# Kernel tuning notes

Hardware: AMD Instinct MI355X
Metric: run time of the kernel (lower is better)

## Reference

```python
import jax, jax.numpy as jnp
import numpy as np

N0, N1, N2 = 200000, 100000, 50000
E0, E1 = 1600000, 800000
IN_F, H_F, N_CLS = 128, 256, 64


def sage_conv(h_src, src_idx, dst_idx, num_dst, W_self, W_neigh, b):
    # DGL SAGEConv with aggregator_type='mean':
    #   h_neigh = mean over in-neighbors of h_src
    #   out = h_dst @ W_self + h_neigh @ W_neigh + b
    h_dst = h_src[:num_dst]
    msgs = h_src[src_idx]                                   # [E, F] gather
    summed = jax.ops.segment_sum(msgs, dst_idx, num_segments=num_dst)
    deg = jax.ops.segment_sum(jnp.ones((src_idx.shape[0],), h_src.dtype),
                              dst_idx, num_segments=num_dst)
    h_neigh = summed / jnp.maximum(deg, 1.0)[:, None]       # mean, safe for deg=0
    return h_dst @ W_self + h_neigh @ W_neigh + b


def setup_inputs() -> dict:
    key = jax.random.key(0)
    ks = jax.random.split(key, 10)
    s1 = 1.0 / np.sqrt(IN_F)
    s2 = 1.0 / np.sqrt(H_F)
    return {
        "x": jax.random.normal(ks[0], (N0, IN_F), jnp.float32),
        "src0": jax.random.randint(ks[1], (E0,), 0, N0, jnp.int64 if jax.config.jax_enable_x64 else jnp.int32),
        "dst0": jnp.sort(jax.random.randint(ks[2], (E0,), 0, N1)),
        "src1": jax.random.randint(ks[3], (E1,), 0, N1),
        "dst1": jnp.sort(jax.random.randint(ks[4], (E1,), 0, N2)),
        "num_dst0": N1,
        "num_dst1": N2,
        "W_self1": jax.random.normal(ks[5], (IN_F, H_F), jnp.float32) * s1,
        "W_neigh1": jax.random.normal(ks[6], (IN_F, H_F), jnp.float32) * s1,
        "b1": jnp.zeros((H_F,), jnp.float32),
        "W_self2": jax.random.normal(ks[7], (H_F, N_CLS), jnp.float32) * s2,
        "W_neigh2": jax.random.normal(ks[8], (H_F, N_CLS), jnp.float32) * s2,
        "b2": jnp.zeros((N_CLS,), jnp.float32),
    }


def reference(x, src0, dst0, src1, dst1, num_dst0, num_dst1,
              W_self1, W_neigh1, b1, W_self2, W_neigh2, b2):
    h = sage_conv(x, src0, dst0, num_dst0, W_self1, W_neigh1, b1)   # [N1, H]
    h = jax.nn.relu(h)
    h = sage_conv(h, src1, dst1, num_dst1, W_self2, W_neigh2, b2)   # [N2, C]
    return h
```

## Files before the change

kernel.cpp:

```cpp
#include <hip/hip_runtime.h>

constexpr int cN0  = 200000;
constexpr int cN1  = 100000;
constexpr int cN2  = 50000;
constexpr int cE0  = 1600000;
constexpr int cE1  = 800000;
constexpr int cIN  = 128;
constexpr int cH   = 256;
constexpr int cCLS = 64;

constexpr float QSTEP = 6.0f / 127.0f;
constexpr float QINV  = 127.0f / 6.0f;

using bf16x8 = __attribute__((ext_vector_type(8))) short;
using f32x4  = __attribute__((ext_vector_type(4))) float;

__device__ __forceinline__ float bflo(unsigned int u) {
    union { unsigned int i; float f; } v; v.i = u << 16; return v.f;
}
__device__ __forceinline__ float bfhi(unsigned int u) {
    union { unsigned int i; float f; } v; v.i = u & 0xFFFF0000u; return v.f;
}
__device__ __forceinline__ unsigned int f2bf(float f) {
    union { float f; unsigned int i; } v; v.f = f;
    return (v.i + 0x7FFFu + ((v.i >> 16) & 1u)) >> 16;
}

constexpr int XBLK = (cN0 * cIN / 8) / 256;
constexpr int WCNT = cH * cH + 2 * cCLS * cH;
constexpr int WBLK = WCNT / 256;
constexpr int RCNT = (cN1 + 1) + (cN2 + 1);
constexpr int RBLK = (RCNT + 255) / 256;

__global__ __launch_bounds__(256) void prep(
        const float* __restrict__ x,
        const float* __restrict__ Ws1, const float* __restrict__ Wn1,
        const float* __restrict__ Wn2, const float* __restrict__ Ws2,
        const int* __restrict__ dst0, const int* __restrict__ dst1,
        unsigned short* __restrict__ xb, unsigned int* __restrict__ xq,
        unsigned short* __restrict__ Wt1, unsigned short* __restrict__ Wt2,
        int* __restrict__ row0, int* __restrict__ row1) {
    const int b = blockIdx.x, tid = threadIdx.x;
    if (b < XBLK) {
        const int i = b * 256 + tid;
        const float4* p = (const float4*)x + (size_t)i * 2;
        float4 a = p[0], c = p[1];
        uint4 o;
        o.x = f2bf(a.x) | (f2bf(a.y) << 16);
        o.y = f2bf(a.z) | (f2bf(a.w) << 16);
        o.z = f2bf(c.x) | (f2bf(c.y) << 16);
        o.w = f2bf(c.z) | (f2bf(c.w) << 16);
        ((uint4*)xb)[i] = o;
        auto q8 = [](float v) -> unsigned int {
            int q = __float2int_rn(v * QINV);
            q = q > 127 ? 127 : (q < -127 ? -127 : q);
            return (unsigned int)q & 255u;
        };
        uint2 d;
        d.x = q8(a.x) | (q8(a.y) << 8) | (q8(a.z) << 16) | (q8(a.w) << 24);
        d.y = q8(c.x) | (q8(c.y) << 8) | (q8(c.z) << 16) | (q8(c.w) << 24);
        ((uint2*)xq)[i] = d;
    } else if (b < XBLK + WBLK) {
        const int wi = (b - XBLK) * 256 + tid;
        if (wi < cH * cH) {
            int n = wi >> 8, k = wi & 255;
            float v = (k < cIN) ? Ws1[k * cH + n] : Wn1[(k - cIN) * cH + n];
            Wt1[n * cH + k] = (unsigned short)f2bf(v);
        } else {
            int j = wi - cH * cH; int n = j >> 8, k = j & 255;
            float v = (n < cCLS) ? Wn2[k * cCLS + n] : Ws2[k * cCLS + (n - cCLS)];
            Wt2[n * cH + k] = (unsigned short)f2bf(v);
        }
    } else {
        const int ti = (b - XBLK - WBLK) * 256 + tid;
        if (ti <= cN1) {
            int lo = 0, hi = cE0;
            while (lo < hi) { int mid = (lo + hi) >> 1; if (dst0[mid] < ti) lo = mid + 1; else hi = mid; }
            row0[ti] = lo;
        } else {
            int d = ti - (cN1 + 1);
            if (d <= cN2) {
                int lo = 0, hi = cE1;
                while (lo < hi) { int mid = (lo + hi) >> 1; if (dst1[mid] < d) lo = mid + 1; else hi = mid; }
                row1[d] = lo;
            }
        }
    }
}

__global__ __launch_bounds__(256) void agg_i8(
        const uint2* __restrict__ xq,
        const int* __restrict__ sidx,
        const int* __restrict__ rows,
        unsigned short* __restrict__ nb,
        int num_dst) {
    const int tid = threadIdx.x, lane = tid & 63;
    const int m = blockIdx.x * 4 + (tid >> 6);
    if (m >= num_dst) return;
    const int sub = lane >> 4, t = lane & 15;
    const int e0 = rows[m], e1 = rows[m + 1];

    int acc[8];
    #pragma unroll
    for (int j = 0; j < 8; ++j) acc[j] = 0;
    auto addq = [&](uint2 v) {
        #pragma unroll
        for (int d = 0; d < 2; ++d) {
            unsigned int w = (&v.x)[d];
            acc[d * 4 + 0] += (int)(signed char)(w);
            acc[d * 4 + 1] += (int)(signed char)(w >> 8);
            acc[d * 4 + 2] += (int)(signed char)(w >> 16);
            acc[d * 4 + 3] += (int)(signed char)(w >> 24);
        }
    };

    int base = e0;
    for (; base + 16 <= e1; base += 16) {
        int sA = sidx[base + sub];
        int sB = sidx[base + 4 + sub];
        int sC = sidx[base + 8 + sub];
        int sD = sidx[base + 12 + sub];
        uint2 vA = xq[(size_t)sA * 16 + t];
        uint2 vB = xq[(size_t)sB * 16 + t];
        uint2 vC = xq[(size_t)sC * 16 + t];
        uint2 vD = xq[(size_t)sD * 16 + t];
        addq(vA); addq(vB); addq(vC); addq(vD);
    }
    for (; base < e1; base += 4) {
        int idx = base + sub;
        if (idx < e1) addq(xq[(size_t)sidx[idx] * 16 + t]);
    }

    #pragma unroll
    for (int j = 0; j < 8; ++j) {
        acc[j] += __shfl_xor(acc[j], 16, 64);
        acc[j] += __shfl_xor(acc[j], 32, 64);
    }

    if (sub == 0) {
        const int deg = e1 - e0;
        const float f = QSTEP / (float)(deg > 1 ? deg : 1);
        uint4 w;
        w.x = f2bf(acc[0] * f) | (f2bf(acc[1] * f) << 16);
        w.y = f2bf(acc[2] * f) | (f2bf(acc[3] * f) << 16);
        w.z = f2bf(acc[4] * f) | (f2bf(acc[5] * f) << 16);
        w.w = f2bf(acc[6] * f) | (f2bf(acc[7] * f) << 16);
        ((uint4*)nb)[(size_t)m * 16 + t] = w;
    }
}

template<int K, bool ACCUM>
__global__ __launch_bounds__(256) void agg_wave(
        const unsigned short* __restrict__ src,
        const int* __restrict__ sidx,
        const int* __restrict__ rows,
        void* __restrict__ outv, int num_dst) {
    constexpr int LPR = K / 8;
    constexpr int EPW = 64 / LPR;
    const int tid = threadIdx.x;
    const int lane = tid & 63;
    const int m = blockIdx.x * 4 + (tid >> 6);
    if (m >= num_dst) return;
    const int sub = lane / LPR;
    const int t   = lane % LPR;

    const uint4* s4 = (const uint4*)src;
    const int e0 = rows[m], e1 = rows[m + 1];

    float acc[8];
    #pragma unroll
    for (int j = 0; j < 8; ++j) acc[j] = 0.f;
    auto addv = [&](uint4 v) {
        acc[0] += bflo(v.x); acc[1] += bfhi(v.x);
        acc[2] += bflo(v.y); acc[3] += bfhi(v.y);
        acc[4] += bflo(v.z); acc[5] += bfhi(v.z);
        acc[6] += bflo(v.w); acc[7] += bfhi(v.w);
    };

    int base = e0;
    for (; base + 2 * EPW <= e1; base += 2 * EPW) {
        int sA = sidx[base + sub], sB = sidx[base + EPW + sub];
        uint4 vA = s4[(size_t)sA * LPR + t];
        uint4 vB = s4[(size_t)sB * LPR + t];
        addv(vA); addv(vB);
    }
    for (; base < e1; base += EPW) {
        int idx = base + sub;
        if (idx < e1) addv(s4[(size_t)sidx[idx] * LPR + t]);
    }

    #pragma unroll
    for (int j = 0; j < 8; ++j) {
        #pragma unroll
        for (int off = LPR; off < 64; off <<= 1)
            acc[j] += __shfl_xor(acc[j], off, 64);
    }

    if (sub == 0) {
        const int deg = e1 - e0;
        const float inv = 1.0f / (float)(deg > 1 ? deg : 1);
        if (!ACCUM) {
            uint4 o;
            o.x = f2bf(acc[0] * inv) | (f2bf(acc[1] * inv) << 16);
            o.y = f2bf(acc[2] * inv) | (f2bf(acc[3] * inv) << 16);
            o.z = f2bf(acc[4] * inv) | (f2bf(acc[5] * inv) << 16);
            o.w = f2bf(acc[6] * inv) | (f2bf(acc[7] * inv) << 16);
            ((uint4*)outv)[(size_t)m * LPR + t] = o;
        } else {
            float* op = (float*)outv + (size_t)m * K + t * 8;
            float4 o0 = *(float4*)op, o1 = *(float4*)(op + 4);
            o0.x += acc[0] * inv; o0.y += acc[1] * inv;
            o0.z += acc[2] * inv; o0.w += acc[3] * inv;
            o1.x += acc[4] * inv; o1.y += acc[5] * inv;
            o1.z += acc[6] * inv; o1.w += acc[7] * inv;
            *(float4*)op = o0; *(float4*)(op + 4) = o1;
        }
    }
}

template<int BM, int BN, int WM, int WN, bool RELU, bool HASBIAS, bool OUTBF16>
__global__ __launch_bounds__(256) void gemm_mfma(
        const unsigned short* __restrict__ A1, int K1,
        const unsigned short* __restrict__ A2, int K2,
        const unsigned short* __restrict__ Bt,
        const float* __restrict__ bias,
        void* __restrict__ Cout, int M, int N) {
    static_assert(2 * WM * 16 == BM && 2 * WN * 16 == BN, "wave tiling");
    __shared__ unsigned short As[BM][40];
    __shared__ unsigned short Bs[BN][40];

    const int tid = threadIdx.x;
    const int m0 = blockIdx.x * BM, n0 = blockIdx.y * BN;
    const int lane = tid & 63, wave = tid >> 6;
    const int wrow = wave >> 1, wcol = wave & 1;
    const int quad = lane >> 4, l16 = lane & 15;
    const int K = K1 + K2;

    f32x4 acc[WM][WN];
    #pragma unroll
    for (int i = 0; i < WM; ++i)
        #pragma unroll
        for (int j = 0; j < WN; ++j)
            acc[i][j] = (f32x4){0.f, 0.f, 0.f, 0.f};

    for (int kb = 0; kb < K; kb += 32) {
        const unsigned short* Ab; int lda, kloc;
        if (kb < K1) { Ab = A1; lda = K1; kloc = kb; }
        else         { Ab = A2; lda = K2; kloc = kb - K1; }

        #pragma unroll
        for (int f = 0; f < (BM * 4) / 256; ++f) {
            int idx = tid + f * 256;
            int row = idx >> 2, q = idx & 3;
            int gm = m0 + row;
            uint4 v = make_uint4(0, 0, 0, 0);
            if (gm < M) v = *(const uint4*)(Ab + (size_t)gm * lda + kloc + q * 8);
            *(uint4*)&As[row][q * 8] = v;
        }
        #pragma unroll
        for (int f = 0; f < (BN * 4) / 256; ++f) {
            int idx = tid + f * 256;
            int row = idx >> 2, q = idx & 3;
            uint4 v = *(const uint4*)(Bt + (size_t)(n0 + row) * K + kb + q * 8);
            *(uint4*)&Bs[row][q * 8] = v;
        }
        __syncthreads();

        bf16x8 a[WM], b[WN];
        #pragma unroll
        for (int i = 0; i < WM; ++i)
            a[i] = *(const bf16x8*)&As[(wrow * WM + i) * 16 + l16][quad * 8];
        #pragma unroll
        for (int j = 0; j < WN; ++j)
            b[j] = *(const bf16x8*)&Bs[(wcol * WN + j) * 16 + l16][quad * 8];
        #pragma unroll
        for (int i = 0; i < WM; ++i)
            #pragma unroll
            for (int j = 0; j < WN; ++j)
                acc[i][j] = __builtin_amdgcn_mfma_f32_16x16x32_bf16(
                    a[i], b[j], acc[i][j], 0, 0, 0);
        __syncthreads();
    }

    float bv[WN];
    #pragma unroll
    for (int j = 0; j < WN; ++j)
        bv[j] = HASBIAS ? bias[n0 + (wcol * WN + j) * 16 + l16] : 0.f;
    #pragma unroll
    for (int i = 0; i < WM; ++i) {
        #pragma unroll
        for (int r = 0; r < 4; ++r) {
            int gm = m0 + (wrow * WM + i) * 16 + quad * 4 + r;
            if (gm >= M) continue;
            #pragma unroll
            for (int j = 0; j < WN; ++j) {
                int gn = n0 + (wcol * WN + j) * 16 + l16;
                float v = acc[i][j][r] + bv[j];
                if (RELU) v = fmaxf(v, 0.f);
                if (OUTBF16)
                    ((unsigned short*)Cout)[(size_t)gm * N + gn] = (unsigned short)f2bf(v);
                else
                    ((float*)Cout)[(size_t)gm * N + gn] = v;
            }
        }
    }
}

__global__ __launch_bounds__(256) void gemm2_split(
        const unsigned short* __restrict__ A,
        const unsigned short* __restrict__ Bt,
        const float* __restrict__ b2,
        unsigned short* __restrict__ zb,
        float* __restrict__ out) {
    __shared__ unsigned short As[128][40];
    __shared__ unsigned short Bs[128][40];
    const int tid = threadIdx.x;
    const int m0 = blockIdx.x * 128;
    const int lane = tid & 63, wave = tid >> 6;
    const int wrow = wave >> 1, wcol = wave & 1;
    const int quad = lane >> 4, l16 = lane & 15;

    f32x4 acc[4][4];
    #pragma unroll
    for (int i = 0; i < 4; ++i)
        #pragma unroll
        for (int j = 0; j < 4; ++j)
            acc[i][j] = (f32x4){0.f, 0.f, 0.f, 0.f};

    for (int kb = 0; kb < cH; kb += 32) {
        #pragma unroll
        for (int f = 0; f < 2; ++f) {
            int idx = tid + f * 256;
            int row = idx >> 2, q = idx & 3;
            int gm = m0 + row;
            uint4 v = make_uint4(0, 0, 0, 0);
            if (gm < cN1) v = *(const uint4*)(A + (size_t)gm * cH + kb + q * 8);
            *(uint4*)&As[row][q * 8] = v;
        }
        #pragma unroll
        for (int f = 0; f < 2; ++f) {
            int idx = tid + f * 256;
            int row = idx >> 2, q = idx & 3;
            uint4 v = *(const uint4*)(Bt + (size_t)row * cH + kb + q * 8);
            *(uint4*)&Bs[row][q * 8] = v;
        }
        __syncthreads();

        bf16x8 a[4], b[4];
        #pragma unroll
        for (int i = 0; i < 4; ++i)
            a[i] = *(const bf16x8*)&As[(wrow * 4 + i) * 16 + l16][quad * 8];
        #pragma unroll
        for (int j = 0; j < 4; ++j)
            b[j] = *(const bf16x8*)&Bs[(wcol * 4 + j) * 16 + l16][quad * 8];
        #pragma unroll
        for (int i = 0; i < 4; ++i)
            #pragma unroll
            for (int j = 0; j < 4; ++j)
                acc[i][j] = __builtin_amdgcn_mfma_f32_16x16x32_bf16(
                    a[i], b[j], acc[i][j], 0, 0, 0);
        __syncthreads();
    }

    if (wcol == 0) {
        #pragma unroll
        for (int i = 0; i < 4; ++i) {
            #pragma unroll
            for (int r = 0; r < 4; ++r) {
                int gm = m0 + (wrow * 4 + i) * 16 + quad * 4 + r;
                if (gm >= cN1) continue;
                #pragma unroll
                for (int j = 0; j < 4; ++j) {
                    int gn = j * 16 + l16;
                    zb[(size_t)gm * cCLS + gn] = (unsigned short)f2bf(acc[i][j][r]);
                }
            }
        }
    } else {
        float bv[4];
        #pragma unroll
        for (int j = 0; j < 4; ++j) bv[j] = b2[j * 16 + l16];
        #pragma unroll
        for (int i = 0; i < 4; ++i) {
            #pragma unroll
            for (int r = 0; r < 4; ++r) {
                int gm = m0 + (wrow * 4 + i) * 16 + quad * 4 + r;
                if (gm >= cN2) continue;
                #pragma unroll
                for (int j = 0; j < 4; ++j)
                    out[(size_t)gm * cCLS + j * 16 + l16] = acc[i][j][r] + bv[j];
            }
        }
    }
}

extern "C" void kernel_launch(void* const* d_in, const int* in_sizes, int n_in,
                              void* d_out, int out_size, void* d_ws, size_t ws_size,
                              hipStream_t stream) {
    const float* x      = (const float*)d_in[0];
    const int*   src0   = (const int*)d_in[1];
    const int*   dst0   = (const int*)d_in[2];
    const int*   src1   = (const int*)d_in[3];
    const int*   dst1   = (const int*)d_in[4];
    const float* Wself1  = (const float*)d_in[7];
    const float* Wneigh1 = (const float*)d_in[8];
    const float* b1      = (const float*)d_in[9];
    const float* Wself2  = (const float*)d_in[10];
    const float* Wneigh2 = (const float*)d_in[11];
    const float* b2      = (const float*)d_in[12];
    float* out = (float*)d_out;

    char* ws = (char*)d_ws;
    int* row0 = (int*)ws;
    int* row1 = row0 + (cN1 + 1);
    size_t off = (size_t)((cN1 + 1) + (cN2 + 1)) * sizeof(int);
    off = (off + 1023) & ~(size_t)1023;
    unsigned short* xb = (unsigned short*)(ws + off); off += (size_t)cN0 * cIN * 2;
    unsigned int*   xq = (unsigned int*)(ws + off);
    unsigned short* zb = (unsigned short*)(ws + off); off += (size_t)cN0 * cIN;
    unsigned short* nb  = (unsigned short*)(ws + off); off += (size_t)cN1 * cIN * 2;
    unsigned short* h1b = (unsigned short*)(ws + off); off += (size_t)cN1 * cH * 2;
    unsigned short* Wt1 = (unsigned short*)(ws + off); off += (size_t)cH * cH * 2;
    unsigned short* Wt2 = (unsigned short*)(ws + off); off += (size_t)2 * cCLS * cH * 2;

    prep<<<XBLK + WBLK + RBLK, 256, 0, stream>>>(
        x, Wself1, Wneigh1, Wneigh2, Wself2, dst0, dst1,
        xb, xq, Wt1, Wt2, row0, row1);

    agg_i8<<<(cN1 + 3) / 4, 256, 0, stream>>>(
        (const uint2*)xq, src0, row0, nb, cN1);

    gemm_mfma<128, 128, 4, 4, true, true, true>
        <<<dim3((cN1 + 127) / 128, cH / 128), 256, 0, stream>>>(
        xb, cIN, nb, cIN, Wt1, b1, h1b, cN1, cH);

    gemm2_split<<<(cN1 + 127) / 128, 256, 0, stream>>>(h1b, Wt2, b2, zb, out);

    agg_wave<cCLS, true><<<(cN2 + 3) / 4, 256, 0, stream>>>(
        zb, src1, row1, out, cN2);
}
```

Measured before the change: 341.1 us.

## Register-prefetch GEMM tiles with K=64 steps and full-N tile for layer-one GEMM

```diff
diff --git a/kernel.cpp b/kernel.cpp
--- a/kernel.cpp
+++ b/kernel.cpp
@@ -218,89 +218,98 @@
     }
 }
 
-template<int BM, int BN, int WM, int WN, bool RELU, bool HASBIAS, bool OUTBF16>
-__global__ __launch_bounds__(256) void gemm_mfma(
-        const unsigned short* __restrict__ A1, int K1,
-        const unsigned short* __restrict__ A2, int K2,
+__global__ __launch_bounds__(256) void gemm1_big(
+        const unsigned short* __restrict__ xb,
+        const unsigned short* __restrict__ nb,
         const unsigned short* __restrict__ Bt,
         const float* __restrict__ bias,
-        void* __restrict__ Cout, int M, int N) {
-    static_assert(2 * WM * 16 == BM && 2 * WN * 16 == BN, "wave tiling");
-    __shared__ unsigned short As[BM][40];
-    __shared__ unsigned short Bs[BN][40];
+        unsigned short* __restrict__ h1b) {
+    __shared__ unsigned short As[128][72];
+    __shared__ unsigned short Bs[256][72];
 
     const int tid = threadIdx.x;
-    const int m0 = blockIdx.x * BM, n0 = blockIdx.y * BN;
+    const int m0 = blockIdx.x * 128;
     const int lane = tid & 63, wave = tid >> 6;
-    const int wrow = wave >> 1, wcol = wave & 1;
+    const int wr = wave >> 1, wc = wave & 1;
     const int quad = lane >> 4, l16 = lane & 15;
-    const int K = K1 + K2;
-
-    f32x4 acc[WM][WN];
-    #pragma unroll
-    for (int i = 0; i < WM; ++i)
-        #pragma unroll
-        for (int j = 0; j < WN; ++j)
+
+    uint4 pa[4], pb[8];
+    auto loadA = [&](int kb) {
+        const unsigned short* base = (kb < 128) ? xb : nb;
+        const int koff = (kb < 128) ? kb : kb - 128;
+        #pragma unroll
+        for (int f = 0; f < 4; ++f) {
+            int idx = tid + f * 256;
+            int row = idx >> 3, c = idx & 7;
+            int gm = m0 + row; if (gm > cN1 - 1) gm = cN1 - 1;
+            pa[f] = *(const uint4*)(base + (size_t)gm * 128 + koff + c * 8);
+        }
+    };
+    auto loadB = [&](int kb) {
+        #pragma unroll
+        for (int f = 0; f < 8; ++f) {
+            int idx = tid + f * 256;
+            int row = idx >> 3, c = idx & 7;
+            pb[f] = *(const uint4*)(Bt + (size_t)row * 256 + kb + c * 8);
+        }
+    };
+    auto store = [&]() {
+        #pragma unroll
+        for (int f = 0; f < 4; ++f) {
+            int idx = tid + f * 256;
+            *(uint4*)&As[idx >> 3][(idx & 7) * 8] = pa[f];
+        }
+        #pragma unroll
+        for (int f = 0; f < 8; ++f) {
+            int idx = tid + f * 256;
+            *(uint4*)&Bs[idx >> 3][(idx & 7) * 8] = pb[f];
+        }
+    };
+
+    f32x4 acc[4][8];
+    #pragma unroll
+    for (int i = 0; i < 4; ++i)
+        #pragma unroll
+        for (int j = 0; j < 8; ++j)
             acc[i][j] = (f32x4){0.f, 0.f, 0.f, 0.f};
 
-    for (int kb = 0; kb < K; kb += 32) {
-        const unsigned short* Ab; int lda, kloc;
-        if (kb < K1) { Ab = A1; lda = K1; kloc = kb; }
-        else         { Ab = A2; lda = K2; kloc = kb - K1; }
-
-        #pragma unroll
-        for (int f = 0; f < (BM * 4) / 256; ++f) {
-            int idx = tid + f * 256;
-            int row = idx >> 2, q = idx & 3;
-            int gm = m0 + row;
-            uint4 v = make_uint4(0, 0, 0, 0);
-            if (gm < M) v = *(const uint4*)(Ab + (size_t)gm * lda + kloc + q * 8);
-            *(uint4*)&As[row][q * 8] = v;
-        }
-        #pragma unroll
-        for (int f = 0; f < (BN * 4) / 256; ++f) {
-            int idx = tid + f * 256;
-            int row = idx >> 2, q = idx & 3;
-            uint4 v = *(const uint4*)(Bt + (size_t)(n0 + row) * K + kb + q * 8);
-            *(uint4*)&Bs[row][q * 8] = v;
-        }
+    loadA(0); loadB(0);
+    for (int it = 0; it < 4; ++it) {
+        store();
         __syncthreads();
-
-        bf16x8 a[WM], b[WN];
-        #pragma unroll
-        for (int i = 0; i < WM; ++i)
-            a[i] = *(const bf16x8*)&As[(wrow * WM + i) * 16 + l16][quad * 8];
-        #pragma unroll
-        for (int j = 0; j < WN; ++j)
-            b[j] = *(const bf16x8*)&Bs[(wcol * WN + j) * 16 + l16][quad * 8];
-        #pragma unroll
-        for (int i = 0; i < WM; ++i)
-            #pragma unroll
-            for (int j = 0; j < WN; ++j)
-                acc[i][j] = __builtin_amdgcn_mfma_f32_16x16x32_bf16(
-                    a[i], b[j], acc[i][j], 0, 0, 0);
+        if (it < 3) { loadA((it + 1) * 64); loadB((it + 1) * 64); }
+        #pragma unroll
+        for (int kk = 0; kk < 2; ++kk) {
+            bf16x8 a[4], b[8];
+            #pragma unroll
+            for (int i = 0; i < 4; ++i)
+                a[i] = *(const bf16x8*)&As[(wr * 4 + i) * 16 + l16][kk * 32 + quad * 8];
+            #pragma unroll
+            for (int j = 0; j < 8; ++j)
+                b[j] = *(const bf16x8*)&Bs[(wc * 8 + j) * 16 + l16][kk * 32 + quad * 8];
+            #pragma unroll
+            for (int i = 0; i < 4; ++i)
+                #pragma unroll
+                for (int j = 0; j < 8; ++j)
+                    acc[i][j] = __builtin_amdgcn_mfma_f32_16x16x32_bf16(
+                        a[i], b[j], acc[i][j], 0, 0, 0);
+        }
         __syncthreads();
     }
 
-    float bv[WN];
-    #pragma unroll
-    for (int j = 0; j < WN; ++j)
-        bv[j] = HASBIAS ? bias[n0 + (wcol * WN + j) * 16 + l16] : 0.f;
-    #pragma unroll
-    for (int i = 0; i < WM; ++i) {
+    float bv[8];
+    #pragma unroll
+    for (int j = 0; j < 8; ++j) bv[j] = bias[(wc * 8 + j) * 16 + l16];
+    #pragma unroll
+    for (int i = 0; i < 4; ++i) {
         #pragma unroll
         for (int r = 0; r < 4; ++r) {
-            int gm = m0 + (wrow * WM + i) * 16 + quad * 4 + r;
-            if (gm >= M) continue;
-            #pragma unroll
-            for (int j = 0; j < WN; ++j) {
-                int gn = n0 + (wcol * WN + j) * 16 + l16;
-                float v = acc[i][j][r] + bv[j];
-                if (RELU) v = fmaxf(v, 0.f);
-                if (OUTBF16)
-                    ((unsigned short*)Cout)[(size_t)gm * N + gn] = (unsigned short)f2bf(v);
-                else
-                    ((float*)Cout)[(size_t)gm * N + gn] = v;
+            int gm = m0 + (wr * 4 + i) * 16 + quad * 4 + r;
+            if (gm >= cN1) continue;
+            #pragma unroll
+            for (int j = 0; j < 8; ++j) {
+                float v = fmaxf(acc[i][j][r] + bv[j], 0.f);
+                h1b[(size_t)gm * 256 + (wc * 8 + j) * 16 + l16] = (unsigned short)f2bf(v);
             }
         }
     }
@@ -312,13 +321,41 @@
         const float* __restrict__ b2,
         unsigned short* __restrict__ zb,
         float* __restrict__ out) {
-    __shared__ unsigned short As[128][40];
-    __shared__ unsigned short Bs[128][40];
+    __shared__ unsigned short As[128][72];
+    __shared__ unsigned short Bs[128][72];
     const int tid = threadIdx.x;
     const int m0 = blockIdx.x * 128;
     const int lane = tid & 63, wave = tid >> 6;
-    const int wrow = wave >> 1, wcol = wave & 1;
+    const int wr = wave >> 1, wc = wave & 1;
     const int quad = lane >> 4, l16 = lane & 15;
+
+    uint4 pa[4], pb[4];
+    auto loadA = [&](int kb) {
+        #pragma unroll
+        for (int f = 0; f < 4; ++f) {
+            int idx = tid + f * 256;
+            int row = idx >> 3, c = idx & 7;
+            int gm = m0 + row; if (gm > cN1 - 1) gm = cN1 - 1;
+            pa[f] = *(const uint4*)(A + (size_t)gm * 256 + kb + c * 8);
+        }
+    };
+    auto loadB = [&](int kb) {
+        #pragma unroll
+        for (int f = 0; f < 4; ++f) {
+            int idx = tid + f * 256;
+            int row = idx >> 3, c = idx & 7;
+            pb[f] = *(const uint4*)(Bt + (size_t)row * 256 + kb + c * 8);
+        }
+    };
+    auto store = [&]() {
+        #pragma unroll
+        for (int f = 0; f < 4; ++f) {
+            int idx = tid + f * 256;
+            *(uint4*)&As[idx >> 3][(idx & 7) * 8] = pa[f];
+            int idx2 = tid + f * 256;
+            *(uint4*)&Bs[idx2 >> 3][(idx2 & 7) * 8] = pb[f];
+        }
+    };
 
     f32x4 acc[4][4];
     #pragma unroll
@@ -327,53 +364,40 @@
         for (int j = 0; j < 4; ++j)
             acc[i][j] = (f32x4){0.f, 0.f, 0.f, 0.f};
 
-    for (int kb = 0; kb < cH; kb += 32) {
-        #pragma unroll
-        for (int f = 0; f < 2; ++f) {
-            int idx = tid + f * 256;
-            int row = idx >> 2, q = idx & 3;
-            int gm = m0 + row;
-            uint4 v = make_uint4(0, 0, 0, 0);
-            if (gm < cN1) v = *(const uint4*)(A + (size_t)gm * cH + kb + q * 8);
-            *(uint4*)&As[row][q * 8] = v;
-        }
-        #pragma unroll
-        for (int f = 0; f < 2; ++f) {
-            int idx = tid + f * 256;
-            int row = idx >> 2, q = idx & 3;
-            uint4 v = *(const uint4*)(Bt + (size_t)row * cH + kb + q * 8);
-            *(uint4*)&Bs[row][q * 8] = v;
-        }
+    loadA(0); loadB(0);
+    for (int it = 0; it < 4; ++it) {
+        store();
         __syncthreads();
-
-        bf16x8 a[4], b[4];
-        #pragma unroll
-        for (int i = 0; i < 4; ++i)
-            a[i] = *(const bf16x8*)&As[(wrow * 4 + i) * 16 + l16][quad * 8];
-        #pragma unroll
-        for (int j = 0; j < 4; ++j)
-            b[j] = *(const bf16x8*)&Bs[(wcol * 4 + j) * 16 + l16][quad * 8];
-        #pragma unroll
-        for (int i = 0; i < 4; ++i)
+        if (it < 3) { loadA((it + 1) * 64); loadB((it + 1) * 64); }
+        #pragma unroll
+        for (int kk = 0; kk < 2; ++kk) {
+            bf16x8 a[4], b[4];
+            #pragma unroll
+            for (int i = 0; i < 4; ++i)
+                a[i] = *(const bf16x8*)&As[(wr * 4 + i) * 16 + l16][kk * 32 + quad * 8];
             #pragma unroll
             for (int j = 0; j < 4; ++j)
-                acc[i][j] = __builtin_amdgcn_mfma_f32_16x16x32_bf16(
-                    a[i], b[j], acc[i][j], 0, 0, 0);
+                b[j] = *(const bf16x8*)&Bs[(wc * 4 + j) * 16 + l16][kk * 32 + quad * 8];
+            #pragma unroll
+            for (int i = 0; i < 4; ++i)
+                #pragma unroll
+                for (int j = 0; j < 4; ++j)
+                    acc[i][j] = __builtin_amdgcn_mfma_f32_16x16x32_bf16(
+                        a[i], b[j], acc[i][j], 0, 0, 0);
+        }
         __syncthreads();
     }
 
-    if (wcol == 0) {
+    if (wc == 0) {
         #pragma unroll
         for (int i = 0; i < 4; ++i) {
             #pragma unroll
             for (int r = 0; r < 4; ++r) {
-                int gm = m0 + (wrow * 4 + i) * 16 + quad * 4 + r;
+                int gm = m0 + (wr * 4 + i) * 16 + quad * 4 + r;
                 if (gm >= cN1) continue;
                 #pragma unroll
-                for (int j = 0; j < 4; ++j) {
-                    int gn = j * 16 + l16;
-                    zb[(size_t)gm * cCLS + gn] = (unsigned short)f2bf(acc[i][j][r]);
-                }
+                for (int j = 0; j < 4; ++j)
+                    zb[(size_t)gm * cCLS + j * 16 + l16] = (unsigned short)f2bf(acc[i][j][r]);
             }
         }
     } else {
@@ -384,7 +408,7 @@
         for (int i = 0; i < 4; ++i) {
             #pragma unroll
             for (int r = 0; r < 4; ++r) {
-                int gm = m0 + (wrow * 4 + i) * 16 + quad * 4 + r;
+                int gm = m0 + (wr * 4 + i) * 16 + quad * 4 + r;
                 if (gm >= cN2) continue;
                 #pragma unroll
                 for (int j = 0; j < 4; ++j)
@@ -430,9 +454,7 @@
     agg_i8<<<(cN1 + 3) / 4, 256, 0, stream>>>(
         (const uint2*)xq, src0, row0, nb, cN1);
 
-    gemm_mfma<128, 128, 4, 4, true, true, true>
-        <<<dim3((cN1 + 127) / 128, cH / 128), 256, 0, stream>>>(
-        xb, cIN, nb, cIN, Wt1, b1, h1b, cN1, cH);
+    gemm1_big<<<(cN1 + 127) / 128, 256, 0, stream>>>(xb, nb, Wt1, b1, h1b);
 
     gemm2_split<<<(cN1 + 127) / 128, 256, 0, stream>>>(h1b, Wt2, b2, zb, out);
 
```

After: 419.4 us. 23.0% more time.

## Prefetch next K-tile into registers in MFMA GEMMs; skip unused bf16 x rows

Applied to the files above, without the earlier changes.

```diff
diff --git a/kernel.cpp b/kernel.cpp
--- a/kernel.cpp
+++ b/kernel.cpp
@@ -45,12 +45,14 @@
         const int i = b * 256 + tid;
         const float4* p = (const float4*)x + (size_t)i * 2;
         float4 a = p[0], c = p[1];
-        uint4 o;
-        o.x = f2bf(a.x) | (f2bf(a.y) << 16);
-        o.y = f2bf(a.z) | (f2bf(a.w) << 16);
-        o.z = f2bf(c.x) | (f2bf(c.y) << 16);
-        o.w = f2bf(c.z) | (f2bf(c.w) << 16);
-        ((uint4*)xb)[i] = o;
+        if ((i >> 4) < cN1) {
+            uint4 o;
+            o.x = f2bf(a.x) | (f2bf(a.y) << 16);
+            o.y = f2bf(a.z) | (f2bf(a.w) << 16);
+            o.z = f2bf(c.x) | (f2bf(c.y) << 16);
+            o.w = f2bf(c.z) | (f2bf(c.w) << 16);
+            ((uint4*)xb)[i] = o;
+        }
         auto q8 = [](float v) -> unsigned int {
             int q = __float2int_rn(v * QINV);
             q = q > 127 ? 127 : (q < -127 ? -127 : q);
@@ -226,6 +228,8 @@
         const float* __restrict__ bias,
         void* __restrict__ Cout, int M, int N) {
     static_assert(2 * WM * 16 == BM && 2 * WN * 16 == BN, "wave tiling");
+    constexpr int AF = (BM * 4) / 256;
+    constexpr int BF = (BN * 4) / 256;
     __shared__ unsigned short As[BM][40];
     __shared__ unsigned short Bs[BN][40];
 
@@ -236,35 +240,53 @@
     const int quad = lane >> 4, l16 = lane & 15;
     const int K = K1 + K2;
 
-    f32x4 acc[WM][WN];
-    #pragma unroll
-    for (int i = 0; i < WM; ++i)
-        #pragma unroll
-        for (int j = 0; j < WN; ++j)
-            acc[i][j] = (f32x4){0.f, 0.f, 0.f, 0.f};
-
-    for (int kb = 0; kb < K; kb += 32) {
+    uint4 pa[AF], pb[BF];
+    auto loadA = [&](int kb) {
         const unsigned short* Ab; int lda, kloc;
         if (kb < K1) { Ab = A1; lda = K1; kloc = kb; }
         else         { Ab = A2; lda = K2; kloc = kb - K1; }
-
-        #pragma unroll
-        for (int f = 0; f < (BM * 4) / 256; ++f) {
+        #pragma unroll
+        for (int f = 0; f < AF; ++f) {
             int idx = tid + f * 256;
             int row = idx >> 2, q = idx & 3;
-            int gm = m0 + row;
-            uint4 v = make_uint4(0, 0, 0, 0);
-            if (gm < M) v = *(const uint4*)(Ab + (size_t)gm * lda + kloc + q * 8);
-            *(uint4*)&As[row][q * 8] = v;
-        }
-        #pragma unroll
-        for (int f = 0; f < (BN * 4) / 256; ++f) {
+            int gm = m0 + row; if (gm > M - 1) gm = M - 1;
+            pa[f] = *(const uint4*)(Ab + (size_t)gm * lda + kloc + q * 8);
+        }
+    };
+    auto loadB = [&](int kb) {
+        #pragma unroll
+        for (int f = 0; f < BF; ++f) {
             int idx = tid + f * 256;
             int row = idx >> 2, q = idx & 3;
-            uint4 v = *(const uint4*)(Bt + (size_t)(n0 + row) * K + kb + q * 8);
-            *(uint4*)&Bs[row][q * 8] = v;
-        }
+            pb[f] = *(const uint4*)(Bt + (size_t)(n0 + row) * K + kb + q * 8);
+        }
+    };
+    auto stage = [&]() {
+        #pragma unroll
+        for (int f = 0; f < AF; ++f) {
+            int idx = tid + f * 256;
+            *(uint4*)&As[idx >> 2][(idx & 3) * 8] = pa[f];
+        }
+        #pragma unroll
+        for (int f = 0; f < BF; ++f) {
+            int idx = tid + f * 256;
+            *(uint4*)&Bs[idx >> 2][(idx & 3) * 8] = pb[f];
+        }
+    };
+
+    f32x4 acc[WM][WN];
+    #pragma unroll
+    for (int i = 0; i < WM; ++i)
+        #pragma unroll
+        for (int j = 0; j < WN; ++j)
+            acc[i][j] = (f32x4){0.f, 0.f, 0.f, 0.f};
+
+    loadA(0); loadB(0);
+    const int NIT = K / 32;
+    for (int it = 0; it < NIT; ++it) {
+        stage();
         __syncthreads();
+        if (it + 1 < NIT) { loadA((it + 1) * 32); loadB((it + 1) * 32); }
 
         bf16x8 a[WM], b[WN];
         #pragma unroll
@@ -320,6 +342,26 @@
     const int wrow = wave >> 1, wcol = wave & 1;
     const int quad = lane >> 4, l16 = lane & 15;
 
+    uint4 pa[2], pb[2];
+    auto loadAB = [&](int kb) {
+        #pragma unroll
+        for (int f = 0; f < 2; ++f) {
+            int idx = tid + f * 256;
+            int row = idx >> 2, q = idx & 3;
+            int gm = m0 + row; if (gm > cN1 - 1) gm = cN1 - 1;
+            pa[f] = *(const uint4*)(A + (size_t)gm * cH + kb + q * 8);
+            pb[f] = *(const uint4*)(Bt + (size_t)row * cH + kb + q * 8);
+        }
+    };
+    auto stage = [&]() {
+        #pragma unroll
+        for (int f = 0; f < 2; ++f) {
+            int idx = tid + f * 256;
+            *(uint4*)&As[idx >> 2][(idx & 3) * 8] = pa[f];
+            *(uint4*)&Bs[idx >> 2][(idx & 3) * 8] = pb[f];
+        }
+    };
+
     f32x4 acc[4][4];
     #pragma unroll
     for (int i = 0; i < 4; ++i)
@@ -327,24 +369,11 @@
         for (int j = 0; j < 4; ++j)
             acc[i][j] = (f32x4){0.f, 0.f, 0.f, 0.f};
 
-    for (int kb = 0; kb < cH; kb += 32) {
-        #pragma unroll
-        for (int f = 0; f < 2; ++f) {
-            int idx = tid + f * 256;
-            int row = idx >> 2, q = idx & 3;
-            int gm = m0 + row;
-            uint4 v = make_uint4(0, 0, 0, 0);
-            if (gm < cN1) v = *(const uint4*)(A + (size_t)gm * cH + kb + q * 8);
-            *(uint4*)&As[row][q * 8] = v;
-        }
-        #pragma unroll
-        for (int f = 0; f < 2; ++f) {
-            int idx = tid + f * 256;
-            int row = idx >> 2, q = idx & 3;
-            uint4 v = *(const uint4*)(Bt + (size_t)row * cH + kb + q * 8);
-            *(uint4*)&Bs[row][q * 8] = v;
-        }
+    loadAB(0);
+    for (int it = 0; it < 8; ++it) {
+        stage();
         __syncthreads();
+        if (it < 7) loadAB((it + 1) * 32);
 
         bf16x8 a[4], b[4];
         #pragma unroll
@@ -370,10 +399,8 @@
                 int gm = m0 + (wrow * 4 + i) * 16 + quad * 4 + r;
                 if (gm >= cN1) continue;
                 #pragma unroll
-                for (int j = 0; j < 4; ++j) {
-                    int gn = j * 16 + l16;
-                    zb[(size_t)gm * cCLS + gn] = (unsigned short)f2bf(acc[i][j][r]);
-                }
+                for (int j = 0; j < 4; ++j)
+                    zb[(size_t)gm * cCLS + j * 16 + l16] = (unsigned short)f2bf(acc[i][j][r]);
             }
         }
     } else {
```

New measurement: 400.0 us. 17.3% more time.
